# Performance work log

Hardware: AMD Instinct MI355X
Metric: run time of the kernel (lower is better)

Reference implementation:

```python
import jax, jax.numpy as jnp
import numpy as np

B, T, D, NH = 2, 2048, 1024, 16


def setup_inputs() -> dict:
    key = jax.random.key(0)
    ks = jax.random.split(key, 9)
    s = 0.02
    return {
        "x": jax.random.normal(ks[0], (B, T, D), jnp.float32),
        "Wq": jax.random.normal(ks[1], (D, D), jnp.float32) * s,
        "bq": jax.random.normal(ks[2], (D,), jnp.float32) * s,
        "Wk": jax.random.normal(ks[3], (D, D), jnp.float32) * s,
        "bk": jax.random.normal(ks[4], (D,), jnp.float32) * s,
        "Wv": jax.random.normal(ks[5], (D, D), jnp.float32) * s,
        "bv": jax.random.normal(ks[6], (D,), jnp.float32) * s,
        "Wp": jax.random.normal(ks[7], (D, D), jnp.float32) * s,
        "bp": jax.random.normal(ks[8], (D,), jnp.float32) * s,
        "num_heads": NH,
    }


def _alibi_slopes(nh):
    # standard ALiBi slopes: 2^(-8*h/nh), h = 1..nh
    return jnp.asarray(2.0 ** (-8.0 * np.arange(1, nh + 1) / nh), jnp.float32)


def reference(x, Wq, bq, Wk, bk, Wv, bv, Wp, bp, num_heads):
    b, t, k = x.shape
    nh = num_heads
    hd = k // nh
    scale = k ** 0.25  # each of q,k divided by k**0.25 -> scores / sqrt(k)

    def split_heads(y):  # [b,t,k] -> [b,nh,t,hd]
        return y.reshape(b, t, nh, hd).transpose(0, 2, 1, 3)

    q = split_heads(x @ Wq.T + bq) / scale
    kk = split_heads(x @ Wk.T + bk) / scale
    v = split_heads(x @ Wv.T + bv)

    scores = jnp.einsum("bhid,bhjd->bhij", q, kk)  # [b,nh,t,t]

    pos = jnp.arange(t)
    rel = pos[None, :] - pos[:, None]  # j - i, <= 0 on causal side
    slopes = _alibi_slopes(nh)
    scores = scores + slopes[None, :, None, None] * rel[None, None, :, :]

    causal = rel <= 0  # [t,t]
    scores = jnp.where(causal[None, None, :, :], scores, -jnp.inf)

    attn = jax.nn.softmax(scores, axis=-1)
    out = jnp.einsum("bhij,bhjd->bhid", attn, v)  # [b,nh,t,hd]
    out = out.transpose(0, 2, 1, 3).reshape(b, t, k)
    return out @ Wp.T + bp
```

## Files before the change

### kernel.cpp

```cpp
#include <hip/hip_runtime.h>


using f32x4  = __attribute__((ext_vector_type(4))) float;
using bf16x8 = __attribute__((ext_vector_type(8))) short;
typedef unsigned short u16;
using u16x4 = __attribute__((ext_vector_type(4))) u16;
using u32x4 = __attribute__((ext_vector_type(4))) unsigned int;

#define T_SEQ  2048
#define NHEAD  16
#define HDIM   64
#define DMODEL 1024
#define MROWS  4096

#define LOG2E 1.4426950408889634f

__device__ __forceinline__ u16 f2bf(float f) {
  union { float f; unsigned u; } v; v.f = f;
  return (u16)((v.u + 0x7fffu + ((v.u >> 16) & 1u)) >> 16);
}

__device__ __forceinline__ unsigned cvt_pk_bf16(float lo, float hi) {
  unsigned r;
  asm("v_cvt_pk_bf16_f32 %0, %1, %2" : "=v"(r) : "v"(lo), "v"(hi));
  return r;
}

__device__ __forceinline__ void gl_lds16(const u16* g, u16* l) {
  __builtin_amdgcn_global_load_lds(
      (const __attribute__((address_space(1))) unsigned int*)g,
      (__attribute__((address_space(3))) unsigned int*)l, 16, 0, 0);
}

__global__ __launch_bounds__(256) void cvt_bf16(const float* __restrict__ src,
                                                u16* __restrict__ dst, int n) {
  int i = (blockIdx.x * 256 + threadIdx.x) * 4;
  if (i < n) {
    const float4 v = *reinterpret_cast<const float4*>(src + i);
    u16x4 o;
    o.x = f2bf(v.x); o.y = f2bf(v.y); o.z = f2bf(v.z); o.w = f2bf(v.w);
    *reinterpret_cast<u16x4*>(dst + i) = o;
  }
}

__global__ __launch_bounds__(256) void cvt_w4(
    const float* __restrict__ w0, const float* __restrict__ w1,
    const float* __restrict__ w2, const float* __restrict__ w3,
    u16* __restrict__ dst) {
  const float* src = (blockIdx.y == 0) ? w0 : (blockIdx.y == 1) ? w1
                   : (blockIdx.y == 2) ? w2 : w3;
  u16* d = dst + (size_t)blockIdx.y * 1048576;
  int i = (blockIdx.x * 256 + threadIdx.x) * 4;
  const float4 v = *reinterpret_cast<const float4*>(src + i);
  u16x4 o;
  o.x = f2bf(v.x); o.y = f2bf(v.y); o.z = f2bf(v.z); o.w = f2bf(v.w);
  *reinterpret_cast<u16x4*>(d + i) = o;
}

__global__ __launch_bounds__(256) void qkv_gemm(
    const u16* __restrict__ xb,
    const u16* __restrict__ wq, const u16* __restrict__ wk, const u16* __restrict__ wv,
    const float* __restrict__ bq, const float* __restrict__ bk, const float* __restrict__ bv,
    u16* __restrict__ q_ws, u16* __restrict__ k_ws, u16* __restrict__ vt_ws)
{
  const int K = DMODEL;
  const int z = blockIdx.z;
  const u16*   W    = (z == 0) ? wq : (z == 1) ? wk : wv;
  const float* bias = (z == 0) ? bq : (z == 1) ? bk : bv;
  const int bm = blockIdx.y, bn = blockIdx.x;
  const int tid = threadIdx.x;
  const int w = tid >> 6, lane = tid & 63, g = lane >> 4, c = lane & 15;
  const int wm = w >> 1, wn = w & 1;

  __shared__ u16 SM[2][2][128][64];

  f32x4 zero4 = {0.f, 0.f, 0.f, 0.f};
  f32x4 acc[4][4];
#pragma unroll
  for (int m = 0; m < 4; ++m)
#pragma unroll
    for (int n = 0; n < 4; ++n) acc[m][n] = zero4;

  int rr[4], cswz[4];
#pragma unroll
  for (int j = 0; j < 4; ++j) {
    int chunk = tid + 256 * j;
    rr[j] = chunk >> 3;
    cswz[j] = ((chunk & 7) ^ (rr[j] & 7)) * 8;
  }

#pragma unroll
  for (int j = 0; j < 4; ++j) {
    int chunk = tid + 256 * j;
    gl_lds16(xb + (size_t)(bm * 128 + rr[j]) * K + cswz[j],
             &SM[0][0][0][0] + chunk * 8);
    gl_lds16(W + (size_t)(bn * 128 + rr[j]) * K + cswz[j],
             &SM[0][1][0][0] + chunk * 8);
  }
  __syncthreads();

  for (int t = 0; t < 16; ++t) {
    const int buf = t & 1;
    if (t < 15) {
      const int k0 = (t + 1) * 64;
#pragma unroll
      for (int j = 0; j < 4; ++j) {
        int chunk = tid + 256 * j;
        gl_lds16(xb + (size_t)(bm * 128 + rr[j]) * K + k0 + cswz[j],
                 &SM[buf ^ 1][0][0][0] + chunk * 8);
        gl_lds16(W + (size_t)(bn * 128 + rr[j]) * K + k0 + cswz[j],
                 &SM[buf ^ 1][1][0][0] + chunk * 8);
      }
    }
#pragma unroll
    for (int kk = 0; kk < 2; ++kk) {
      bf16x8 af[4], bfr[4];
#pragma unroll
      for (int m = 0; m < 4; ++m) {
        int row = wm * 64 + m * 16 + c;
        af[m] = *reinterpret_cast<const bf16x8*>(
            &SM[buf][0][row][(kk * 32 + g * 8) ^ ((row & 7) * 8)]);
      }
#pragma unroll
      for (int n = 0; n < 4; ++n) {
        int row = wn * 64 + n * 16 + c;
        bfr[n] = *reinterpret_cast<const bf16x8*>(
            &SM[buf][1][row][(kk * 32 + g * 8) ^ ((row & 7) * 8)]);
      }
#pragma unroll
      for (int m = 0; m < 4; ++m)
#pragma unroll
        for (int n = 0; n < 4; ++n)
          acc[m][n] = __builtin_amdgcn_mfma_f32_16x16x32_bf16(af[m], bfr[n], acc[m][n], 0, 0, 0);
    }
    __syncthreads();
  }

  const float rs = 0.1767766953f;
  const float qs = rs * LOG2E;

  if (z == 2) {
    u16* tr = &SM[0][0][0][0];
    const int bb = (bm * 128) >> 11;
    const int t_base = (bm * 128) & (T_SEQ - 1);
#pragma unroll
    for (int hh = 0; hh < 2; ++hh) {
      __syncthreads();
      if (wn == hh) {
#pragma unroll
        for (int n = 0; n < 4; ++n) {
          float bv_ = bias[bn * 128 + wn * 64 + n * 16 + c];
#pragma unroll
          for (int m = 0; m < 4; ++m) {
#pragma unroll
            for (int i = 0; i < 4; ++i) {
              tr[(n * 16 + c) * 136 + wm * 64 + m * 16 + g * 4 + i] =
                  f2bf(acc[m][n][i] + bv_);
            }
          }
        }
      }
      __syncthreads();
#pragma unroll
      for (int rep = 0; rep < 4; ++rep) {
        int idx = tid + rep * 256;
        int dr = idx >> 4, ch = idx & 15;
        bf16x8 vv = *reinterpret_cast<const bf16x8*>(&tr[dr * 136 + ch * 8]);
        int d_glob = bn * 128 + hh * 64 + dr;
        int head = d_glob >> 6, dd = d_glob & 63;
        *reinterpret_cast<bf16x8*>(
            vt_ws + (((size_t)(bb * NHEAD + head) * HDIM + dd) * T_SEQ) + t_base + ch * 8) = vv;
      }
    }
  } else {
    u16* dst = (z == 0) ? q_ws : k_ws;
    const float sc = (z == 0) ? qs : rs;
#pragma unroll
    for (int m = 0; m < 4; ++m) {
      int mrow_base = bm * 128 + wm * 64 + m * 16 + g * 4;
#pragma unroll
      for (int n = 0; n < 4; ++n) {
        int n_idx = bn * 128 + wn * 64 + n * 16 + c;
        float bv_ = bias[n_idx];
        int head = n_idx >> 6, d = n_idx & 63;
#pragma unroll
        for (int i = 0; i < 4; ++i) {
          int mrow = mrow_base + i;
          int b = mrow >> 11, t = mrow & (T_SEQ - 1);
          dst[((size_t)(b * NHEAD + head) * T_SEQ + t) * HDIM + d] =
              f2bf((acc[m][n][i] + bv_) * sc);
        }
      }
    }
  }
}

__global__ __launch_bounds__(256, 4) void attn_fused(
    const u16* __restrict__ Q, const u16* __restrict__ Kk,
    const u16* __restrict__ VT, u16* __restrict__ O)
{
  const int tid = threadIdx.x;
  const int w = tid >> 6;
  const int lane = tid & 63;
  const int g = lane >> 4, c = lane & 15;
  const int j = blockIdx.x;
  const int bh = blockIdx.y;
  const int h = bh & (NHEAD - 1), b = bh >> 4;
  const float slope2 = exp2f(-0.5f * (float)(h + 1)) * LOG2E;
  const u16* Qp = Q  + (size_t)bh * T_SEQ * HDIM;
  const u16* Kp = Kk + (size_t)bh * T_SEQ * HDIM;
  const u16* Vp = VT + (size_t)bh * HDIM * T_SEQ;

  __shared__ u16 KB[2][64][64];
  __shared__ u16 VB[2][64][64];

  const int s_r0 = tid >> 3;
  const int s_r1 = s_r0 + 32;
  const int s_c0 = ((tid & 7) ^ (s_r0 & 7)) * 8;

  f32x4 zero4 = {0.f, 0.f, 0.f, 0.f};

  for (int pass = 0; pass < 2; ++pass) {
    const int qb = (pass == 0) ? (T_SEQ / 64 - 1 - j) : j;
    const int q0 = qb * 64;
    const int qrow = q0 + w * 16;
    const int nt = qb + 1;

    bf16x8 qf0 = *reinterpret_cast<const bf16x8*>(Qp + (size_t)(qrow + c) * HDIM + g * 8);
    bf16x8 qf1 = *reinterpret_cast<const bf16x8*>(Qp + (size_t)(qrow + c) * HDIM + 32 + g * 8);

    {
      u16* kb = &KB[0][0][0]; u16* vb = &VB[0][0][0];
      gl_lds16(Kp + (size_t)(q0 + s_r0) * HDIM + s_c0, kb + tid * 8);
      gl_lds16(Kp + (size_t)(q0 + s_r1) * HDIM + s_c0, kb + (tid + 256) * 8);
      gl_lds16(Vp + (size_t)s_r0 * T_SEQ + q0 + s_c0, vb + tid * 8);
      gl_lds16(Vp + (size_t)s_r1 * T_SEQ + q0 + s_c0, vb + (tid + 256) * 8);
    }
    __syncthreads();

    f32x4 o[4];
#pragma unroll
    for (int dg = 0; dg < 4; ++dg) o[dg] = zero4;
    float mrun = -3.0e38f, lrun = 0.f;

    for (int t = 0; t < nt; ++t) {
      const u16* kb = &KB[t & 1][0][0];
      const u16* vb = &VB[t & 1][0][0];

      if (t + 1 < nt) {
        const int kvn = (nt - 2 - t) * 64;
        u16* kbn = &KB[(t + 1) & 1][0][0];
        u16* vbn = &VB[(t + 1) & 1][0][0];
        gl_lds16(Kp + (size_t)(kvn + s_r0) * HDIM + s_c0, kbn + tid * 8);
        gl_lds16(Kp + (size_t)(kvn + s_r1) * HDIM + s_c0, kbn + (tid + 256) * 8);
        gl_lds16(Vp + (size_t)s_r0 * T_SEQ + kvn + s_c0, vbn + tid * 8);
        gl_lds16(Vp + (size_t)s_r1 * T_SEQ + kvn + s_c0, vbn + (tid + 256) * 8);
      }

      const int kv0 = (nt - 1 - t) * 64;

      f32x4 s[4];
#pragma unroll
      for (int jj = 0; jj < 4; ++jj) {
        const int r = jj * 16 + c;
        bf16x8 k0 = *reinterpret_cast<const bf16x8*>(kb + r * 64 + ((g ^ (r & 7)) * 8));
        bf16x8 k1 = *reinterpret_cast<const bf16x8*>(kb + r * 64 + (((4 + g) ^ (r & 7)) * 8));
        f32x4 z4 = zero4;
        z4 = __builtin_amdgcn_mfma_f32_16x16x32_bf16(k0, qf0, z4, 0, 0, 0);
        z4 = __builtin_amdgcn_mfma_f32_16x16x32_bf16(k1, qf1, z4, 0, 0, 0);
        s[jj] = z4;
      }

      const int kbase = kv0 + 4 * g - (qrow + c);
      float mt = -3.0e38f;
      if (t == 0) {
#pragma unroll
        for (int jj = 0; jj < 4; ++jj)
#pragma unroll
          for (int i = 0; i < 4; ++i) {
            int rel = kbase + 16 * jj + i;
            float sv = s[jj][i] + slope2 * (float)rel;
            if (rel > 0) sv = -3.0e38f;
            s[jj][i] = sv;
            mt = fmaxf(mt, sv);
          }
      } else {
#pragma unroll
        for (int jj = 0; jj < 4; ++jj)
#pragma unroll
          for (int i = 0; i < 4; ++i) {
            float sv = s[jj][i] + slope2 * (float)(kbase + 16 * jj + i);
            s[jj][i] = sv;
            mt = fmaxf(mt, sv);
          }
      }
      mt = fmaxf(mt, __shfl_xor(mt, 16, 64));
      mt = fmaxf(mt, __shfl_xor(mt, 32, 64));

      if (!__all(mt <= mrun + 11.5416f)) {
        float mnew = fmaxf(mrun, mt);
        float alpha = __builtin_amdgcn_exp2f(mrun - mnew);
        mrun = mnew;
        lrun *= alpha;
        float ar[4];
#pragma unroll
        for (int i = 0; i < 4; ++i) ar[i] = __shfl(alpha, g * 4 + i, 64);
#pragma unroll
        for (int dg = 0; dg < 4; ++dg)
#pragma unroll
          for (int i = 0; i < 4; ++i) o[dg][i] *= ar[i];
      }

      float p[16];
      float rsum = 0.f;
#pragma unroll
      for (int jj = 0; jj < 4; ++jj)
#pragma unroll
        for (int i = 0; i < 4; ++i) {
          float e = __builtin_amdgcn_exp2f(s[jj][i] - mrun);
          rsum += e;
          p[jj * 4 + i] = e;
        }
      union { bf16x8 v; u32x4 u; } P0, P1;
#pragma unroll
      for (int k = 0; k < 4; ++k) {
        P0.u[k] = cvt_pk_bf16(p[2 * k], p[2 * k + 1]);
        P1.u[k] = cvt_pk_bf16(p[8 + 2 * k], p[8 + 2 * k + 1]);
      }
      rsum += __shfl_xor(rsum, 16, 64);
      rsum += __shfl_xor(rsum, 32, 64);
      lrun += rsum;

#pragma unroll
      for (int dg = 0; dg < 4; ++dg) {
        const int vr = dg * 16 + c;
        const int vbase = vr * 64 + (g & 1) * 4;
        const int sw = vr & 7;
        short4 a0 = *reinterpret_cast<const short4*>(vb + vbase + (((g >> 1) + 0) ^ sw) * 8);
        short4 a1 = *reinterpret_cast<const short4*>(vb + vbase + (((g >> 1) + 2) ^ sw) * 8);
        short4 a2 = *reinterpret_cast<const short4*>(vb + vbase + (((g >> 1) + 4) ^ sw) * 8);
        short4 a3 = *reinterpret_cast<const short4*>(vb + vbase + (((g >> 1) + 6) ^ sw) * 8);
        bf16x8 vf0, vf1;
#pragma unroll
        for (int e = 0; e < 4; ++e) {
          vf0[e] = a0[e]; vf0[4 + e] = a1[e];
          vf1[e] = a2[e]; vf1[4 + e] = a3[e];
        }
        o[dg] = __builtin_amdgcn_mfma_f32_16x16x32_bf16(P0.v, vf0, o[dg], 0, 0, 0);
        o[dg] = __builtin_amdgcn_mfma_f32_16x16x32_bf16(P1.v, vf1, o[dg], 0, 0, 0);
      }

      __syncthreads();
    }

    float rl[4];
#pragma unroll
    for (int i = 0; i < 4; ++i) {
      float li = __shfl(lrun, g * 4 + i, 64);
      rl[i] = 1.0f / li;
    }
#pragma unroll
    for (int dg = 0; dg < 4; ++dg) {
#pragma unroll
      for (int i = 0; i < 4; ++i) {
        int qi = qrow + g * 4 + i;
        O[((size_t)b * T_SEQ + qi) * DMODEL + h * HDIM + dg * 16 + c] =
            f2bf(o[dg][i] * rl[i]);
      }
    }
  }
}

__global__ __launch_bounds__(256) void out_gemm(
    const u16* __restrict__ ao, const u16* __restrict__ wp,
    const float* __restrict__ bp, float* __restrict__ out)
{
  const int K = DMODEL;
  const int bm = blockIdx.y, bn = blockIdx.x;
  const int tid = threadIdx.x;
  const int w = tid >> 6, lane = tid & 63, g = lane >> 4, c = lane & 15;
  const int wm = w >> 1, wn = w & 1;

  __shared__ u16 SM[2][2][128][64];

  f32x4 zero4 = {0.f, 0.f, 0.f, 0.f};
  f32x4 acc[4][4];
#pragma unroll
  for (int m = 0; m < 4; ++m)
#pragma unroll
    for (int n = 0; n < 4; ++n) acc[m][n] = zero4;

  int rr[4], cswz[4];
#pragma unroll
  for (int j = 0; j < 4; ++j) {
    int chunk = tid + 256 * j;
    rr[j] = chunk >> 3;
    cswz[j] = ((chunk & 7) ^ (rr[j] & 7)) * 8;
  }

#pragma unroll
  for (int j = 0; j < 4; ++j) {
    int chunk = tid + 256 * j;
    gl_lds16(ao + (size_t)(bm * 128 + rr[j]) * K + cswz[j],
             &SM[0][0][0][0] + chunk * 8);
    gl_lds16(wp + (size_t)(bn * 128 + rr[j]) * K + cswz[j],
             &SM[0][1][0][0] + chunk * 8);
  }
  __syncthreads();

  for (int t = 0; t < 16; ++t) {
    const int buf = t & 1;
    if (t < 15) {
      const int k0 = (t + 1) * 64;
#pragma unroll
      for (int j = 0; j < 4; ++j) {
        int chunk = tid + 256 * j;
        gl_lds16(ao + (size_t)(bm * 128 + rr[j]) * K + k0 + cswz[j],
                 &SM[buf ^ 1][0][0][0] + chunk * 8);
        gl_lds16(wp + (size_t)(bn * 128 + rr[j]) * K + k0 + cswz[j],
                 &SM[buf ^ 1][1][0][0] + chunk * 8);
      }
    }
#pragma unroll
    for (int kk = 0; kk < 2; ++kk) {
      bf16x8 af[4], bfr[4];
#pragma unroll
      for (int m = 0; m < 4; ++m) {
        int row = wm * 64 + m * 16 + c;
        af[m] = *reinterpret_cast<const bf16x8*>(
            &SM[buf][0][row][(kk * 32 + g * 8) ^ ((row & 7) * 8)]);
      }
#pragma unroll
      for (int n = 0; n < 4; ++n) {
        int row = wn * 64 + n * 16 + c;
        bfr[n] = *reinterpret_cast<const bf16x8*>(
            &SM[buf][1][row][(kk * 32 + g * 8) ^ ((row & 7) * 8)]);
      }
#pragma unroll
      for (int m = 0; m < 4; ++m)
#pragma unroll
        for (int n = 0; n < 4; ++n)
          acc[m][n] = __builtin_amdgcn_mfma_f32_16x16x32_bf16(af[m], bfr[n], acc[m][n], 0, 0, 0);
    }
    __syncthreads();
  }

#pragma unroll
  for (int m = 0; m < 4; ++m) {
    int mrow_base = bm * 128 + wm * 64 + m * 16 + g * 4;
#pragma unroll
    for (int n = 0; n < 4; ++n) {
      int n_idx = bn * 128 + wn * 64 + n * 16 + c;
      float bv_ = bp[n_idx];
#pragma unroll
      for (int i = 0; i < 4; ++i) {
        int mrow = mrow_base + i;
        out[(size_t)mrow * DMODEL + n_idx] = acc[m][n][i] + bv_;
      }
    }
  }
}

extern "C" void kernel_launch(void* const* d_in, const int* in_sizes, int n_in,
                              void* d_out, int out_size, void* d_ws, size_t ws_size,
                              hipStream_t stream) {
  const float* x  = (const float*)d_in[0];
  const float* Wq = (const float*)d_in[1];
  const float* bq = (const float*)d_in[2];
  const float* Wk = (const float*)d_in[3];
  const float* bk = (const float*)d_in[4];
  const float* Wv = (const float*)d_in[5];
  const float* bv = (const float*)d_in[6];
  const float* Wp = (const float*)d_in[7];
  const float* bp = (const float*)d_in[8];
  float* out = (float*)d_out;

  u16* ws    = (u16*)d_ws;
  u16* xb    = ws;
  u16* wqb   = xb   + 4194304;
  u16* wkb   = wqb  + 1048576;
  u16* wvb   = wkb  + 1048576;
  u16* wpb   = wvb  + 1048576;
  u16* q_ws  = wpb  + 1048576;
  u16* k_ws  = q_ws + 4194304;
  u16* vt_ws = k_ws + 4194304;
  u16* ao    = vt_ws + 4194304;

  cvt_bf16<<<4096, 256, 0, stream>>>(x, xb, 4194304);
  cvt_w4<<<dim3(1024, 4), 256, 0, stream>>>(Wq, Wk, Wv, Wp, wqb);

  qkv_gemm<<<dim3(DMODEL / 128, MROWS / 128, 3), 256, 0, stream>>>(
      xb, wqb, wkb, wvb, bq, bk, bv, q_ws, k_ws, vt_ws);

  attn_fused<<<dim3(T_SEQ / 128, 2 * NHEAD), 256, 0, stream>>>(q_ws, k_ws, vt_ws, ao);

  out_gemm<<<dim3(DMODEL / 128, MROWS / 128), 256, 0, stream>>>(ao, wpb, bp, out);
}
```

Measured before the change: 121.2 us.

## Triple-buffer K/V tiles in attention with one barrier per iteration

```diff
diff --git a/kernel.cpp b/kernel.cpp
--- a/kernel.cpp
+++ b/kernel.cpp
@@ -195,7 +195,7 @@
   }
 }
 
-__global__ __launch_bounds__(256, 4) void attn_fused(
+__global__ __launch_bounds__(256) void attn_fused(
     const u16* __restrict__ Q, const u16* __restrict__ Kk,
     const u16* __restrict__ VT, u16* __restrict__ O)
 {
@@ -211,12 +211,19 @@
   const u16* Kp = Kk + (size_t)bh * T_SEQ * HDIM;
   const u16* Vp = VT + (size_t)bh * HDIM * T_SEQ;
 
-  __shared__ u16 KB[2][64][64];
-  __shared__ u16 VB[2][64][64];
+  __shared__ u16 KB[3][64][64];
+  __shared__ u16 VB[3][64][64];
 
   const int s_r0 = tid >> 3;
   const int s_r1 = s_r0 + 32;
   const int s_c0 = ((tid & 7) ^ (s_r0 & 7)) * 8;
+
+  auto stage = [&](int kv, int buf) {
+    gl_lds16(Kp + (size_t)(kv + s_r0) * HDIM + s_c0, &KB[buf][0][0] + tid * 8);
+    gl_lds16(Kp + (size_t)(kv + s_r1) * HDIM + s_c0, &KB[buf][0][0] + (tid + 256) * 8);
+    gl_lds16(Vp + (size_t)s_r0 * T_SEQ + kv + s_c0, &VB[buf][0][0] + tid * 8);
+    gl_lds16(Vp + (size_t)s_r1 * T_SEQ + kv + s_c0, &VB[buf][0][0] + (tid + 256) * 8);
+  };
 
   f32x4 zero4 = {0.f, 0.f, 0.f, 0.f};
 
@@ -229,14 +236,12 @@
     bf16x8 qf0 = *reinterpret_cast<const bf16x8*>(Qp + (size_t)(qrow + c) * HDIM + g * 8);
     bf16x8 qf1 = *reinterpret_cast<const bf16x8*>(Qp + (size_t)(qrow + c) * HDIM + 32 + g * 8);
 
-    {
-      u16* kb = &KB[0][0][0]; u16* vb = &VB[0][0][0];
-      gl_lds16(Kp + (size_t)(q0 + s_r0) * HDIM + s_c0, kb + tid * 8);
-      gl_lds16(Kp + (size_t)(q0 + s_r1) * HDIM + s_c0, kb + (tid + 256) * 8);
-      gl_lds16(Vp + (size_t)s_r0 * T_SEQ + q0 + s_c0, vb + tid * 8);
-      gl_lds16(Vp + (size_t)s_r1 * T_SEQ + q0 + s_c0, vb + (tid + 256) * 8);
-    }
-    __syncthreads();
+    asm volatile("s_waitcnt vmcnt(0)" ::: "memory");
+    __builtin_amdgcn_s_barrier();
+    __builtin_amdgcn_sched_barrier(0);
+
+    stage(q0, 0);
+    stage(nt > 1 ? q0 - 64 : q0, 1);
 
     f32x4 o[4];
 #pragma unroll
@@ -244,19 +249,14 @@
     float mrun = -3.0e38f, lrun = 0.f;
 
     for (int t = 0; t < nt; ++t) {
-      const u16* kb = &KB[t & 1][0][0];
-      const u16* vb = &VB[t & 1][0][0];
-
-      if (t + 1 < nt) {
-        const int kvn = (nt - 2 - t) * 64;
-        u16* kbn = &KB[(t + 1) & 1][0][0];
-        u16* vbn = &VB[(t + 1) & 1][0][0];
-        gl_lds16(Kp + (size_t)(kvn + s_r0) * HDIM + s_c0, kbn + tid * 8);
-        gl_lds16(Kp + (size_t)(kvn + s_r1) * HDIM + s_c0, kbn + (tid + 256) * 8);
-        gl_lds16(Vp + (size_t)s_r0 * T_SEQ + kvn + s_c0, vbn + tid * 8);
-        gl_lds16(Vp + (size_t)s_r1 * T_SEQ + kvn + s_c0, vbn + (tid + 256) * 8);
-      }
-
+      asm volatile("s_waitcnt vmcnt(4)" ::: "memory");
+      __builtin_amdgcn_s_barrier();
+      __builtin_amdgcn_sched_barrier(0);
+
+      stage((t + 2 < nt) ? (nt - 3 - t) * 64 : q0, (t + 2) % 3);
+
+      const u16* kb = &KB[t % 3][0][0];
+      const u16* vb = &VB[t % 3][0][0];
       const int kv0 = (nt - 1 - t) * 64;
 
       f32x4 s[4];
@@ -349,8 +349,6 @@
         o[dg] = __builtin_amdgcn_mfma_f32_16x16x32_bf16(P0.v, vf0, o[dg], 0, 0, 0);
         o[dg] = __builtin_amdgcn_mfma_f32_16x16x32_bf16(P1.v, vf1, o[dg], 0, 0, 0);
       }
-
-      __syncthreads();
     }
 
     float rl[4];
```

Result: slower. 124.3 us (+2.6%).

## Split attention into 32-row two-wave blocks with head-interleaved 1D grid

Applied to the files above, without the earlier changes.

```diff
diff --git a/kernel.cpp b/kernel.cpp
--- a/kernel.cpp
+++ b/kernel.cpp
@@ -195,7 +195,7 @@
   }
 }
 
-__global__ __launch_bounds__(256, 4) void attn_fused(
+__global__ __launch_bounds__(128, 2) void attn_fused(
     const u16* __restrict__ Q, const u16* __restrict__ Kk,
     const u16* __restrict__ VT, u16* __restrict__ O)
 {
@@ -203,8 +203,10 @@
   const int w = tid >> 6;
   const int lane = tid & 63;
   const int g = lane >> 4, c = lane & 15;
-  const int j = blockIdx.x;
-  const int bh = blockIdx.y;
+  const int bid = blockIdx.x;
+  const int inner = bid >> 3;
+  const int bh = (bid & 7) + 8 * (inner & 3);
+  const int j = inner >> 2;
   const int h = bh & (NHEAD - 1), b = bh >> 4;
   const float slope2 = exp2f(-0.5f * (float)(h + 1)) * LOG2E;
   const u16* Qp = Q  + (size_t)bh * T_SEQ * HDIM;
@@ -214,27 +216,29 @@
   __shared__ u16 KB[2][64][64];
   __shared__ u16 VB[2][64][64];
 
-  const int s_r0 = tid >> 3;
-  const int s_r1 = s_r0 + 32;
-  const int s_c0 = ((tid & 7) ^ (s_r0 & 7)) * 8;
+  const int s_rb = tid >> 3;
+  const int s_c0q = (tid & 7);
 
   f32x4 zero4 = {0.f, 0.f, 0.f, 0.f};
 
   for (int pass = 0; pass < 2; ++pass) {
-    const int qb = (pass == 0) ? (T_SEQ / 64 - 1 - j) : j;
-    const int q0 = qb * 64;
+    const int qb = (pass == 0) ? (63 - j) : j;
+    const int q0 = qb * 32;
     const int qrow = q0 + w * 16;
-    const int nt = qb + 1;
+    const int nt = (qb >> 1) + 1;
 
     bf16x8 qf0 = *reinterpret_cast<const bf16x8*>(Qp + (size_t)(qrow + c) * HDIM + g * 8);
     bf16x8 qf1 = *reinterpret_cast<const bf16x8*>(Qp + (size_t)(qrow + c) * HDIM + 32 + g * 8);
 
     {
-      u16* kb = &KB[0][0][0]; u16* vb = &VB[0][0][0];
-      gl_lds16(Kp + (size_t)(q0 + s_r0) * HDIM + s_c0, kb + tid * 8);
-      gl_lds16(Kp + (size_t)(q0 + s_r1) * HDIM + s_c0, kb + (tid + 256) * 8);
-      gl_lds16(Vp + (size_t)s_r0 * T_SEQ + q0 + s_c0, vb + tid * 8);
-      gl_lds16(Vp + (size_t)s_r1 * T_SEQ + q0 + s_c0, vb + (tid + 256) * 8);
+      const int kv0 = (nt - 1) * 64;
+#pragma unroll
+      for (int sw = 0; sw < 4; ++sw) {
+        int r = s_rb + 16 * sw;
+        int cs = ((s_c0q ^ (r & 7)) * 8);
+        gl_lds16(Kp + (size_t)(kv0 + r) * HDIM + cs, &KB[0][0][0] + (tid + 128 * sw) * 8);
+        gl_lds16(Vp + (size_t)r * T_SEQ + kv0 + cs, &VB[0][0][0] + (tid + 128 * sw) * 8);
+      }
     }
     __syncthreads();
 
@@ -251,10 +255,13 @@
         const int kvn = (nt - 2 - t) * 64;
         u16* kbn = &KB[(t + 1) & 1][0][0];
         u16* vbn = &VB[(t + 1) & 1][0][0];
-        gl_lds16(Kp + (size_t)(kvn + s_r0) * HDIM + s_c0, kbn + tid * 8);
-        gl_lds16(Kp + (size_t)(kvn + s_r1) * HDIM + s_c0, kbn + (tid + 256) * 8);
-        gl_lds16(Vp + (size_t)s_r0 * T_SEQ + kvn + s_c0, vbn + tid * 8);
-        gl_lds16(Vp + (size_t)s_r1 * T_SEQ + kvn + s_c0, vbn + (tid + 256) * 8);
+#pragma unroll
+        for (int sw = 0; sw < 4; ++sw) {
+          int r = s_rb + 16 * sw;
+          int cs = ((s_c0q ^ (r & 7)) * 8);
+          gl_lds16(Kp + (size_t)(kvn + r) * HDIM + cs, kbn + (tid + 128 * sw) * 8);
+          gl_lds16(Vp + (size_t)r * T_SEQ + kvn + cs, vbn + (tid + 128 * sw) * 8);
+        }
       }
 
       const int kv0 = (nt - 1 - t) * 64;
@@ -271,9 +278,10 @@
         s[jj] = z4;
       }
 
-      const int kbase = kv0 + 4 * g - (qrow + c);
+      const float biasbase = slope2 * (float)(kv0 + 4 * g - (qrow + c));
       float mt = -3.0e38f;
       if (t == 0) {
+        const int kbase = kv0 + 4 * g - (qrow + c);
 #pragma unroll
         for (int jj = 0; jj < 4; ++jj)
 #pragma unroll
@@ -289,15 +297,15 @@
         for (int jj = 0; jj < 4; ++jj)
 #pragma unroll
           for (int i = 0; i < 4; ++i) {
-            float sv = s[jj][i] + slope2 * (float)(kbase + 16 * jj + i);
+            float sv = s[jj][i] + (biasbase + slope2 * (float)(16 * jj + i));
             s[jj][i] = sv;
             mt = fmaxf(mt, sv);
           }
       }
-      mt = fmaxf(mt, __shfl_xor(mt, 16, 64));
-      mt = fmaxf(mt, __shfl_xor(mt, 32, 64));
 
       if (!__all(mt <= mrun + 11.5416f)) {
+        mt = fmaxf(mt, __shfl_xor(mt, 16, 64));
+        mt = fmaxf(mt, __shfl_xor(mt, 32, 64));
         float mnew = fmaxf(mrun, mt);
         float alpha = __builtin_amdgcn_exp2f(mrun - mnew);
         mrun = mnew;
@@ -327,8 +335,6 @@
         P0.u[k] = cvt_pk_bf16(p[2 * k], p[2 * k + 1]);
         P1.u[k] = cvt_pk_bf16(p[8 + 2 * k], p[8 + 2 * k + 1]);
       }
-      rsum += __shfl_xor(rsum, 16, 64);
-      rsum += __shfl_xor(rsum, 32, 64);
       lrun += rsum;
 
 #pragma unroll
@@ -353,6 +359,8 @@
       __syncthreads();
     }
 
+    lrun += __shfl_xor(lrun, 16, 64);
+    lrun += __shfl_xor(lrun, 32, 64);
     float rl[4];
 #pragma unroll
     for (int i = 0; i < 4; ++i) {
@@ -368,6 +376,7 @@
             f2bf(o[dg][i] * rl[i]);
       }
     }
+    __syncthreads();
   }
 }
 
@@ -492,7 +501,7 @@
   qkv_gemm<<<dim3(DMODEL / 128, MROWS / 128, 3), 256, 0, stream>>>(
       xb, wqb, wkb, wvb, bq, bk, bv, q_ws, k_ws, vt_ws);
 
-  attn_fused<<<dim3(T_SEQ / 128, 2 * NHEAD), 256, 0, stream>>>(q_ws, k_ws, vt_ws, ao);
+  attn_fused<<<1024, 128, 0, stream>>>(q_ws, k_ws, vt_ws, ao);
 
   out_gemm<<<dim3(DMODEL / 128, MROWS / 128), 256, 0, stream>>>(ao, wpb, bp, out);
 }
```

Result: no change. 119.8 us (-1.1%).
